# Kernel optimization log

Measured on AMD Instinct MI355X. Metric: run time of the kernel, lower is better.

The kernel has to match this reference:

```python
import jax, jax.numpy as jnp
import numpy as np


def _dwconv3d(x, w, b):
    # depthwise Conv3d, kernel 3, stride 1, padding 1 (SAME), groups = channels
    groups = x.shape[1]
    y = jax.lax.conv_general_dilated(
        x, w, window_strides=(1, 1, 1), padding='SAME',
        feature_group_count=groups,
        dimension_numbers=('NCDHW', 'OIDHW', 'NCDHW'))
    return y + b[None, :, None, None, None]


def setup_inputs() -> dict:
    key = jax.random.key(0)
    ks = jax.random.split(key, 8)
    B, C, K, D, H, W = 4, 64, 64, 16, 64, 64
    sc = 0.1
    return {
        'x_q': jax.random.normal(ks[0], (B, C, D, H, W), jnp.float32),
        'x_kv': jax.random.normal(ks[1], (B, K, D, H, W), jnp.float32),
        'wq': jax.random.normal(ks[2], (C, 1, 3, 3, 3), jnp.float32) * sc,
        'bq': jax.random.normal(ks[3], (C,), jnp.float32) * sc,
        'wk': jax.random.normal(ks[4], (K, 1, 3, 3, 3), jnp.float32) * sc,
        'bk': jax.random.normal(ks[5], (K,), jnp.float32) * sc,
        'wv': jax.random.normal(ks[6], (K, 1, 3, 3, 3), jnp.float32) * sc,
        'bv': jax.random.normal(ks[7], (K,), jnp.float32) * sc,
    }


def reference(x_q, x_kv, wq, bq, wk, bk, wv, bv):
    q = _dwconv3d(x_q, wq, bq)   # [B,C,D,H,W]
    k = _dwconv3d(x_kv, wk, bk)  # [B,K,D,H,W]
    v = _dwconv3d(x_kv, wv, bv)  # [B,K,D,H,W]
    B, C = q.shape[:2]
    K = k.shape[1]
    qf = q.reshape(B, C, -1)     # [B,C,S]
    kf = k.reshape(B, K, -1)     # [B,K,S]
    vf = v.reshape(B, K, -1)     # [B,K,S]
    attn = jnp.einsum('bcs,bks->bck', qf, kf) / jnp.sqrt(jnp.asarray(K, qf.dtype))
    attn = jax.nn.softmax(attn, axis=-1)           # [B,C,K]
    n = int(0.1 * C)
    at = attn.transpose(0, 2, 1)                   # [B,K,C]
    _, idx = jax.lax.top_k(at, n)                  # [B,K,n] indices into C
    mask = jnp.sum(jax.nn.one_hot(idx, C, dtype=attn.dtype), axis=-2)  # [B,K,C]
    attn_m = attn * mask.transpose(0, 2, 1)        # [B,C,K], NOT renormalized
    out = jnp.einsum('bck,bks->bcs', attn_m, vf).reshape(q.shape)
    return x_q + out, attn_m
```

## Files before the change

### kernel.cpp

```cpp
#include <hip/hip_runtime.h>
#include <math.h>

#define BB   4
#define CC   64
#define KK   64
#define DDim 16
#define HDim 64
#define WDim 64
#define SS   (DDim*HDim*WDim)
#define PLANE (HDim*WDim)
#define NCH2 64
#define TOPN 6
#define RSTR 68
#define RROWS 18
#define NSTG 288

typedef __attribute__((ext_vector_type(8))) short bf16x8;
typedef __attribute__((ext_vector_type(4))) float f32x4;

__device__ __forceinline__ unsigned cvt_pk_bf16(float lo, float hi) {
    unsigned r;
    asm("v_cvt_pk_bf16_f32 %0, %1, %2" : "=v"(r) : "v"(lo), "v"(hi));
    return r;
}
__device__ __forceinline__ float bf2f(unsigned short u) {
    union { unsigned u; float f; } v; v.u = ((unsigned)u) << 16; return v.f;
}

__global__ __launch_bounds__(128) void conv_hp4(
    const float* __restrict__ xq, const float* __restrict__ xkv,
    const float* __restrict__ wq, const float* __restrict__ bq,
    const float* __restrict__ wk, const float* __restrict__ bk,
    const float* __restrict__ wv, const float* __restrict__ bv,
    unsigned short* __restrict__ qo, unsigned short* __restrict__ ko,
    unsigned short* __restrict__ vo)
{
    __shared__ float ring[4][RROWS*RSTR];

    int bid  = blockIdx.x;
    int work = (bid & 7) * 256 + (bid >> 3);
    int t  = work >> 10;
    int b  = (work >> 8) & 3;
    int c  = (work >> 2) & 63;
    int hs = work & 3;
    int g0 = hs << 4;

    const float* src = (t ? xkv : xq) + (size_t)(b*CC + c) * SS;
    float wA[27], wB[27], bA, bB;
    if (t == 0) {
        #pragma unroll
        for (int i = 0; i < 27; ++i) { wA[i] = wq[c*27 + i]; wB[i] = 0.f; }
        bA = bq[c]; bB = 0.f;
    } else {
        #pragma unroll
        for (int i = 0; i < 27; ++i) { wA[i] = wk[c*27 + i]; wB[i] = wv[c*27 + i]; }
        bA = bk[c]; bB = bv[c];
    }
    unsigned short* dA = (t ? ko : qo) + (size_t)(b*CC + c) * SS;
    unsigned short* dB = vo + (size_t)(b*CC + c) * SS;

    const int tid  = threadIdx.x;
    const int lane = tid & 63;
    const int wg   = tid & 7;
    const int w0   = wg << 3;
    const int hl   = tid >> 3;
    const int y    = g0 + hl;

    float4 stg[3];
#define SLOAD(p) {                                                             \
    const int p_ = (p);                                                        \
    const bool pv_ = (p_ >= 0 && p_ < DDim);                                   \
    _Pragma("unroll")                                                          \
    for (int i_ = 0; i_ < 3; ++i_) {                                           \
        const int fidx_ = i_*128 + tid;                                        \
        const int row_  = fidx_ >> 4;                                          \
        const int gy_   = g0 - 1 + row_;                                       \
        float4 v_ = make_float4(0.f,0.f,0.f,0.f);                              \
        if (pv_ && fidx_ < NSTG && gy_ >= 0 && gy_ < HDim)                     \
            v_ = *(const float4*)(src + (size_t)p_*PLANE + gy_*WDim            \
                                  + (fidx_ & 15)*4);                           \
        stg[i_] = v_;                                                          \
    } }
#define SWRITE(p) {                                                            \
    float* R_ = ring[(p) & 3];                                                 \
    _Pragma("unroll")                                                          \
    for (int i_ = 0; i_ < 3; ++i_) {                                           \
        const int fidx_ = i_*128 + tid;                                        \
        if (fidx_ < NSTG)                                                      \
            *(float4*)&R_[(fidx_ >> 4)*RSTR + (fidx_ & 15)*4] = stg[i_];       \
    } }

#define COMPUTE_D(dd, DOB) {                                                   \
    float accA[8], accB[8];                                                    \
    _Pragma("unroll")                                                          \
    for (int j = 0; j < 8; ++j) { accA[j] = bA; accB[j] = bB; }                \
    _Pragma("unroll")                                                          \
    for (int dz = 0; dz < 3; ++dz) {                                           \
        const float* R = ring[((dd) + dz + 3) & 3];         \
        _Pragma("unroll")                                                      \
        for (int dy = 0; dy < 3; ++dy) {                                       \
            const int base_ = (hl + dy)*RSTR;                                  \
            float4 a0 = *(const float4*)&R[base_ + w0];                        \
            float4 a1 = *(const float4*)&R[base_ + w0 + 4];                    \
            float lh = __shfl(a1.w, lane - 1, 64);        \
            float rh = __shfl(a0.x, lane + 1, 64);       \
            float r[10];                                                       \
            r[0] = wg       ? lh : 0.f;                                        \
            r[9] = (wg < 7) ? rh : 0.f;                                        \
            r[1]=a0.x; r[2]=a0.y; r[3]=a0.z; r[4]=a0.w;                        \
            r[5]=a1.x; r[6]=a1.y; r[7]=a1.z; r[8]=a1.w;                        \
            const float ca0 = wA[dz*9 + dy*3 + 0];                             \
            const float ca1 = wA[dz*9 + dy*3 + 1];                             \
            const float ca2 = wA[dz*9 + dy*3 + 2];                             \
            const float cb0 = wB[dz*9 + dy*3 + 0];                             \
            const float cb1 = wB[dz*9 + dy*3 + 1];                             \
            const float cb2 = wB[dz*9 + dy*3 + 2];                             \
            _Pragma("unroll")                                                  \
            for (int j = 0; j < 8; ++j) {                                      \
                float sA = fmaf(ca0, r[j],   accA[j]);                         \
                sA       = fmaf(ca1, r[j+1], sA);                              \
                accA[j]  = fmaf(ca2, r[j+2], sA);                              \
                if (DOB) {                                                     \
                    float sB = fmaf(cb0, r[j],   accB[j]);                     \
                    sB       = fmaf(cb1, r[j+1], sB);                          \
                    accB[j]  = fmaf(cb2, r[j+2], sB);                          \
                }                                                              \
            }                                                                  \
        }                                                                      \
    }                                                                          \
    const int off = (dd)*PLANE + y*WDim + w0;                                  \
    uint2 pkA;                                                                 \
    pkA.x = cvt_pk_bf16(accA[0], accA[1]);                                     \
    pkA.y = cvt_pk_bf16(accA[2], accA[3]);                                     \
    uint2 pkA2;                                                                \
    pkA2.x = cvt_pk_bf16(accA[4], accA[5]);                                    \
    pkA2.y = cvt_pk_bf16(accA[6], accA[7]);                                    \
    *(uint2*)&dA[off]     = pkA;                                               \
    *(uint2*)&dA[off + 4] = pkA2;                                              \
    if (DOB) {                                                                 \
        uint2 pkB, pkB2;                                                       \
        pkB.x  = cvt_pk_bf16(accB[0], accB[1]);                                \
        pkB.y  = cvt_pk_bf16(accB[2], accB[3]);                                \
        pkB2.x = cvt_pk_bf16(accB[4], accB[5]);                                \
        pkB2.y = cvt_pk_bf16(accB[6], accB[7]);                                \
        *(uint2*)&dB[off]     = pkB;                                           \
        *(uint2*)&dB[off + 4] = pkB2;                                          \
    } }

    SLOAD(-1); SWRITE(-1);
    SLOAD(0);  SWRITE(0);
    SLOAD(1);  SWRITE(1);
    __syncthreads();

    if (t == 0) {
        for (int d = 0; d < DDim; ++d) {
            if (d < DDim - 1) SLOAD(d + 2);
            COMPUTE_D(d, 0);
            if (d < DDim - 1) SWRITE(d + 2);
            __syncthreads();
        }
    } else {
        for (int d = 0; d < DDim; ++d) {
            if (d < DDim - 1) SLOAD(d + 2);
            COMPUTE_D(d, 1);
            if (d < DDim - 1) SWRITE(d + 2);
            __syncthreads();
        }
    }
#undef SLOAD
#undef SWRITE
#undef COMPUTE_D
}

__global__ __launch_bounds__(256) void gemm1_mfma(
    const unsigned short* __restrict__ qb, const unsigned short* __restrict__ kb,
    float* __restrict__ part)
{
    __shared__ unsigned short lq[64*136];
    __shared__ unsigned short lk[64*136];

    int bid   = blockIdx.x;
    int b     = bid >> 6;
    int chunk = bid & 63;
    int tid   = threadIdx.x;
    int lane  = tid & 63;
    int wid   = tid >> 6;
    int c0    = wid << 4;
    int lr    = lane & 15;
    int kq    = lane >> 4;

    const unsigned short* qsrc = qb + (size_t)b*CC*SS;
    const unsigned short* ksrc = kb + (size_t)b*KK*SS;

    f32x4 acc[4];
    #pragma unroll
    for (int j = 0; j < 4; ++j) acc[j] = (f32x4){0.f, 0.f, 0.f, 0.f};

    const int sbase = chunk << 10;
    for (int sc = 0; sc < 8; ++sc) {
        const int s0 = sbase + (sc << 7);
        __syncthreads();
        #pragma unroll
        for (int it = 0; it < 8; ++it) {
            const int idx  = it*256 + tid;
            const int tile = idx >> 10;
            const int row  = (idx >> 4) & 63;
            const int ch8  = idx & 15;
            const unsigned short* s_ = (tile ? ksrc : qsrc) + (size_t)row*SS + s0 + ch8*8;
            unsigned short* d_ = (tile ? lk : lq) + row*136 + ch8*8;
            *(uint4*)d_ = *(const uint4*)s_;
        }
        __syncthreads();
        #pragma unroll
        for (int ss = 0; ss < 4; ++ss) {
            const int scol = ss*32 + kq*8;
            bf16x8 a = *(const bf16x8*)&lq[(c0 + lr)*136 + scol];
            #pragma unroll
            for (int j = 0; j < 4; ++j) {
                bf16x8 bv = *(const bf16x8*)&lk[(j*16 + lr)*136 + scol];
                acc[j] = __builtin_amdgcn_mfma_f32_16x16x32_bf16(a, bv, acc[j], 0, 0, 0);
            }
        }
    }

    float* pb = part + ((size_t)(b*NCH2 + chunk)) * (CC*KK);
    #pragma unroll
    for (int j = 0; j < 4; ++j)
        #pragma unroll
        for (int r = 0; r < 4; ++r)
            pb[(c0 + kq*4 + r)*KK + j*16 + lr] = acc[j][r];
}

__global__ __launch_bounds__(256) void reduce_attn(
    const float* __restrict__ part, float* __restrict__ attn)
{
    int bid = blockIdx.x;
    int b = bid >> 6, c = bid & 63;
    int tid = threadIdx.x;
    int k = tid & 63, g = tid >> 6;
    float s = 0.f;
    for (int ch = g; ch < NCH2; ch += 4)
        s += part[(size_t)(b*NCH2 + ch)*(CC*KK) + c*KK + k];
    __shared__ float red[256];
    red[tid] = s;
    __syncthreads();
    if (tid < 64) {
        float tot = red[tid] + red[tid+64] + red[tid+128] + red[tid+192];
        attn[b*CC*KK + c*KK + tid] = tot * 0.125f;
    }
}

__global__ __launch_bounds__(64) void softmax_topk(
    const float* __restrict__ attn, float* __restrict__ attn_m)
{
    __shared__ float p[64*65];
    int b = blockIdx.x;
    int t = threadIdx.x;
    for (int i = 0; i < 64; ++i) p[i*65 + t] = attn[b*4096 + i*64 + t];
    __syncthreads();
    float m = -1e30f;
    for (int k = 0; k < 64; ++k) m = fmaxf(m, p[t*65 + k]);
    float sum = 0.f;
    for (int k = 0; k < 64; ++k) { float e = expf(p[t*65+k] - m); p[t*65+k] = e; sum += e; }
    float inv = 1.f / sum;
    for (int k = 0; k < 64; ++k) p[t*65+k] *= inv;
    __syncthreads();
    unsigned long long chosen = 0ull;
    #pragma unroll
    for (int pass = 0; pass < TOPN; ++pass) {
        float best = -1.f; int bi = 0;
        for (int c2 = 0; c2 < 64; ++c2) {
            float v = p[c2*65 + t];
            if (!((chosen >> c2) & 1ull) && v > best) { best = v; bi = c2; }
        }
        chosen |= 1ull << bi;
    }
    for (int c2 = 0; c2 < 64; ++c2) {
        float v = p[c2*65 + t];
        attn_m[b*4096 + c2*64 + t] = ((chosen >> c2) & 1ull) ? v : 0.f;
    }
}

__global__ __launch_bounds__(256) void gemm2_out(
    const float* __restrict__ attn_m, const unsigned short* __restrict__ v,
    const float* __restrict__ xq, float* __restrict__ out)
{
    __shared__ float amt[64][68];
    __shared__ float vt[64][132];
    int bid = blockIdx.x;
    int b  = bid >> 7;
    int ch = bid & 127;
    int tid = threadIdx.x;
    for (int i = 0; i < 16; ++i) {
        int idx = i*256 + tid;
        amt[idx & 63][idx >> 6] = attn_m[b*4096 + idx];
    }
    int c0 = (tid >> 4) * 4;
    int s0 = (tid & 15) * 8;
    const unsigned short* vb = v + (size_t)b*KK*SS;
    const float* xb = xq + (size_t)b*CC*SS;
    float* ob = out + (size_t)b*CC*SS;
    int sb0 = ch * 512;
    for (int st = 0; st < 4; ++st) {
        int sb = sb0 + st*128;
        __syncthreads();
        #pragma unroll
        for (int i = 0; i < 4; ++i) {
            int idx = i*256 + tid;
            int k   = idx >> 4;
            int s8  = (idx & 15) * 8;
            uint4 pk = *(const uint4*)&vb[(size_t)k*SS + sb + s8];
            float* dst = &vt[k][s8];
            dst[0] = bf2f((unsigned short)(pk.x & 0xffff));
            dst[1] = bf2f((unsigned short)(pk.x >> 16));
            dst[2] = bf2f((unsigned short)(pk.y & 0xffff));
            dst[3] = bf2f((unsigned short)(pk.y >> 16));
            dst[4] = bf2f((unsigned short)(pk.z & 0xffff));
            dst[5] = bf2f((unsigned short)(pk.z >> 16));
            dst[6] = bf2f((unsigned short)(pk.w & 0xffff));
            dst[7] = bf2f((unsigned short)(pk.w >> 16));
        }
        __syncthreads();
        float acc[4][8] = {};
        #pragma unroll 8
        for (int k = 0; k < 64; ++k) {
            float4 a  = *(const float4*)&amt[k][c0];
            float4 v0 = *(const float4*)&vt[k][s0];
            float4 v1 = *(const float4*)&vt[k][s0+4];
            float av[4] = {a.x,a.y,a.z,a.w};
            float vv[8] = {v0.x,v0.y,v0.z,v0.w,v1.x,v1.y,v1.z,v1.w};
            #pragma unroll
            for (int i = 0; i < 4; ++i)
                #pragma unroll
                for (int j = 0; j < 8; ++j)
                    acc[i][j] = fmaf(av[i], vv[j], acc[i][j]);
        }
        #pragma unroll
        for (int i = 0; i < 4; ++i) {
            int off = (c0+i)*SS + sb + s0;
            float4 x0 = *(const float4*)&xb[off];
            float4 x1 = *(const float4*)&xb[off+4];
            *(float4*)&ob[off]   = make_float4(acc[i][0]+x0.x, acc[i][1]+x0.y,
                                               acc[i][2]+x0.z, acc[i][3]+x0.w);
            *(float4*)&ob[off+4] = make_float4(acc[i][4]+x1.x, acc[i][5]+x1.y,
                                               acc[i][6]+x1.z, acc[i][7]+x1.w);
        }
    }
}

extern "C" void kernel_launch(void* const* d_in, const int* in_sizes, int n_in,
                              void* d_out, int out_size, void* d_ws, size_t ws_size,
                              hipStream_t stream)
{
    const float* xq  = (const float*)d_in[0];
    const float* xkv = (const float*)d_in[1];
    const float* wq  = (const float*)d_in[2];
    const float* bq  = (const float*)d_in[3];
    const float* wk  = (const float*)d_in[4];
    const float* bk  = (const float*)d_in[5];
    const float* wv  = (const float*)d_in[6];
    const float* bv  = (const float*)d_in[7];
    float* out = (float*)d_out;

    unsigned short* k_ws = (unsigned short*)d_ws;
    unsigned short* v_ws = k_ws + (size_t)BB*KK*SS;
    float* part = (float*)(v_ws + (size_t)BB*KK*SS);
    float* attn = part + (size_t)BB*NCH2*CC*KK;

    unsigned short* q_bf = (unsigned short*)out;
    float* attn_m = out + (size_t)BB*CC*SS;

    conv_hp4   <<<2*BB*CC*4, 128, 0, stream>>>(xq, xkv, wq, bq, wk, bk, wv, bv,
                                               q_bf, k_ws, v_ws);
    gemm1_mfma <<<BB*NCH2,   256, 0, stream>>>(q_bf, k_ws, part);
    reduce_attn<<<BB*CC,     256, 0, stream>>>(part, attn);
    softmax_topk<<<BB,        64, 0, stream>>>(attn, attn_m);
    gemm2_out  <<<BB*128,    256, 0, stream>>>(attn_m, v_ws, xq, out);
}
```

Measured before the change: 146.2 us.

## Merge Q and KV depthwise conv blocks into one uniform block per tile

Each block now convolves both the x_q and x_kv tiles for the same (b, c, h-slab), producing q, k and v together. This replaces the two block types of different cost, where q blocks did one conv and kv blocks did two, with one uniform block that halves the grid and balances work across blocks. In exchange it doubles the LDS ring per block and raises register pressure from the three accumulators and three weight sets, which may lower occupancy. It also issues wider 16-byte bf16 stores.

After: 139.9 us (median of 2 runs). 4.3% less time.

```diff
diff --git a/kernel.cpp b/kernel.cpp
--- a/kernel.cpp
+++ b/kernel.cpp
@@ -27,7 +27,7 @@
     union { unsigned u; float f; } v; v.u = ((unsigned)u) << 16; return v.f;
 }
 
-__global__ __launch_bounds__(128) void conv_hp4(
+__global__ __launch_bounds__(128) void conv_uni(
     const float* __restrict__ xq, const float* __restrict__ xkv,
     const float* __restrict__ wq, const float* __restrict__ bq,
     const float* __restrict__ wk, const float* __restrict__ bk,
@@ -35,29 +35,30 @@
     unsigned short* __restrict__ qo, unsigned short* __restrict__ ko,
     unsigned short* __restrict__ vo)
 {
-    __shared__ float ring[4][RROWS*RSTR];
+    __shared__ float ringQ[4][RROWS*RSTR];
+    __shared__ float ringK[4][RROWS*RSTR];
 
     int bid  = blockIdx.x;
-    int work = (bid & 7) * 256 + (bid >> 3);
-    int t  = work >> 10;
-    int b  = (work >> 8) & 3;
+    int work = (bid & 7) * 128 + (bid >> 3);
+    int b  = work >> 8;
     int c  = (work >> 2) & 63;
-    int hs = work & 3;
-    int g0 = hs << 4;
-
-    const float* src = (t ? xkv : xq) + (size_t)(b*CC + c) * SS;
-    float wA[27], wB[27], bA, bB;
-    if (t == 0) {
-        #pragma unroll
-        for (int i = 0; i < 27; ++i) { wA[i] = wq[c*27 + i]; wB[i] = 0.f; }
-        bA = bq[c]; bB = 0.f;
-    } else {
-        #pragma unroll
-        for (int i = 0; i < 27; ++i) { wA[i] = wk[c*27 + i]; wB[i] = wv[c*27 + i]; }
-        bA = bk[c]; bB = bv[c];
-    }
-    unsigned short* dA = (t ? ko : qo) + (size_t)(b*CC + c) * SS;
-    unsigned short* dB = vo + (size_t)(b*CC + c) * SS;
+    int hq = work & 3;
+    int g0 = hq << 4;
+
+    const float* srcQ = xq  + (size_t)(b*CC + c) * SS;
+    const float* srcK = xkv + (size_t)(b*CC + c) * SS;
+    float wQ[27], wK[27], wV[27];
+    #pragma unroll
+    for (int i = 0; i < 27; ++i) {
+        wQ[i] = wq[c*27 + i];
+        wK[i] = wk[c*27 + i];
+        wV[i] = wv[c*27 + i];
+    }
+    const float bQ = bq[c], bK = bk[c], bV = bv[c];
+
+    unsigned short* dQ = qo + (size_t)(b*CC + c) * SS;
+    unsigned short* dK = ko + (size_t)(b*CC + c) * SS;
+    unsigned short* dV = vo + (size_t)(b*CC + c) * SS;
 
     const int tid  = threadIdx.x;
     const int lane = tid & 63;
@@ -66,8 +67,8 @@
     const int hl   = tid >> 3;
     const int y    = g0 + hl;
 
-    float4 stg[3];
-#define SLOAD(p) {                                                             \
+    float4 stgQ[3], stgK[3];
+#define SLOAD2(p) {                                                            \
     const int p_ = (p);                                                        \
     const bool pv_ = (p_ >= 0 && p_ < DDim);                                   \
     _Pragma("unroll")                                                          \
@@ -75,100 +76,110 @@
         const int fidx_ = i_*128 + tid;                                        \
         const int row_  = fidx_ >> 4;                                          \
         const int gy_   = g0 - 1 + row_;                                       \
-        float4 v_ = make_float4(0.f,0.f,0.f,0.f);                              \
-        if (pv_ && fidx_ < NSTG && gy_ >= 0 && gy_ < HDim)                     \
-            v_ = *(const float4*)(src + (size_t)p_*PLANE + gy_*WDim            \
-                                  + (fidx_ & 15)*4);                           \
-        stg[i_] = v_;                                                          \
+        float4 vq_ = make_float4(0.f,0.f,0.f,0.f), vk_ = vq_;                  \
+        if (pv_ && fidx_ < NSTG && gy_ >= 0 && gy_ < HDim) {                   \
+            const size_t o_ = (size_t)p_*PLANE + gy_*WDim + (fidx_ & 15)*4;    \
+            vq_ = *(const float4*)(srcQ + o_);                                 \
+            vk_ = *(const float4*)(srcK + o_);                                 \
+        }                                                                      \
+        stgQ[i_] = vq_; stgK[i_] = vk_;                                        \
     } }
-#define SWRITE(p) {                                                            \
-    float* R_ = ring[(p) & 3];                                                 \
+#define SWRITE2(p) {                                                           \
+    float* RQ_ = ringQ[(p) & 3];                                               \
+    float* RK_ = ringK[(p) & 3];                                               \
     _Pragma("unroll")                                                          \
     for (int i_ = 0; i_ < 3; ++i_) {                                           \
         const int fidx_ = i_*128 + tid;                                        \
-        if (fidx_ < NSTG)                                                      \
-            *(float4*)&R_[(fidx_ >> 4)*RSTR + (fidx_ & 15)*4] = stg[i_];       \
+        if (fidx_ < NSTG) {                                                    \
+            const int off_ = (fidx_ >> 4)*RSTR + (fidx_ & 15)*4;               \
+            *(float4*)&RQ_[off_] = stgQ[i_];                                   \
+            *(float4*)&RK_[off_] = stgK[i_];                                   \
+        }                                                                      \
     } }
 
-#define COMPUTE_D(dd, DOB) {                                                   \
-    float accA[8], accB[8];                                                    \
+#define COMPUTE_D(dd) {                                                        \
+    float accQ[8], accK[8], accV[8];                                           \
     _Pragma("unroll")                                                          \
-    for (int j = 0; j < 8; ++j) { accA[j] = bA; accB[j] = bB; }                \
+    for (int j = 0; j < 8; ++j) { accQ[j] = bQ; accK[j] = bK; accV[j] = bV; }  \
     _Pragma("unroll")                                                          \
     for (int dz = 0; dz < 3; ++dz) {                                           \
-        const float* R = ring[((dd) + dz + 3) & 3];         \
+        const float* RQ = ringQ[((dd) + dz + 3) & 3];       \
+        const float* RK = ringK[((dd) + dz + 3) & 3];                          \
         _Pragma("unroll")                                                      \
         for (int dy = 0; dy < 3; ++dy) {                                       \
             const int base_ = (hl + dy)*RSTR;                                  \
-            float4 a0 = *(const float4*)&R[base_ + w0];                        \
-            float4 a1 = *(const float4*)&R[base_ + w0 + 4];                    \
-            float lh = __shfl(a1.w, lane - 1, 64);        \
-            float rh = __shfl(a0.x, lane + 1, 64);       \
-            float r[10];                                                       \
-            r[0] = wg       ? lh : 0.f;                                        \
-            r[9] = (wg < 7) ? rh : 0.f;                                        \
-            r[1]=a0.x; r[2]=a0.y; r[3]=a0.z; r[4]=a0.w;                        \
-            r[5]=a1.x; r[6]=a1.y; r[7]=a1.z; r[8]=a1.w;                        \
-            const float ca0 = wA[dz*9 + dy*3 + 0];                             \
-            const float ca1 = wA[dz*9 + dy*3 + 1];                             \
-            const float ca2 = wA[dz*9 + dy*3 + 2];                             \
-            const float cb0 = wB[dz*9 + dy*3 + 0];                             \
-            const float cb1 = wB[dz*9 + dy*3 + 1];                             \
-            const float cb2 = wB[dz*9 + dy*3 + 2];                             \
+            float4 qa0 = *(const float4*)&RQ[base_ + w0];                      \
+            float4 qa1 = *(const float4*)&RQ[base_ + w0 + 4];                  \
+            float4 ka0 = *(const float4*)&RK[base_ + w0];                      \
+            float4 ka1 = *(const float4*)&RK[base_ + w0 + 4];                  \
+            float qlh = __shfl(qa1.w, lane - 1, 64);                           \
+            float qrh = __shfl(qa0.x, lane + 1, 64);                           \
+            float klh = __shfl(ka1.w, lane - 1, 64);                           \
+            float krh = __shfl(ka0.x, lane + 1, 64);                           \
+            float rq[10], rk[10];                                              \
+            rq[0] = wg       ? qlh : 0.f;                                      \
+            rq[9] = (wg < 7) ? qrh : 0.f;                                      \
+            rq[1]=qa0.x; rq[2]=qa0.y; rq[3]=qa0.z; rq[4]=qa0.w;                \
+            rq[5]=qa1.x; rq[6]=qa1.y; rq[7]=qa1.z; rq[8]=qa1.w;                \
+            rk[0] = wg       ? klh : 0.f;                                      \
+            rk[9] = (wg < 7) ? krh : 0.f;                                      \
+            rk[1]=ka0.x; rk[2]=ka0.y; rk[3]=ka0.z; rk[4]=ka0.w;                \
+            rk[5]=ka1.x; rk[6]=ka1.y; rk[7]=ka1.z; rk[8]=ka1.w;                \
+            const float cq0 = wQ[dz*9 + dy*3 + 0];                             \
+            const float cq1 = wQ[dz*9 + dy*3 + 1];                             \
+            const float cq2 = wQ[dz*9 + dy*3 + 2];                             \
+            const float ck0 = wK[dz*9 + dy*3 + 0];                             \
+            const float ck1 = wK[dz*9 + dy*3 + 1];                             \
+            const float ck2 = wK[dz*9 + dy*3 + 2];                             \
+            const float cv0 = wV[dz*9 + dy*3 + 0];                             \
+            const float cv1 = wV[dz*9 + dy*3 + 1];                             \
+            const float cv2 = wV[dz*9 + dy*3 + 2];                             \
             _Pragma("unroll")                                                  \
             for (int j = 0; j < 8; ++j) {                                      \
-                float sA = fmaf(ca0, r[j],   accA[j]);                         \
-                sA       = fmaf(ca1, r[j+1], sA);                              \
-                accA[j]  = fmaf(ca2, r[j+2], sA);                              \
-                if (DOB) {                                                     \
-                    float sB = fmaf(cb0, r[j],   accB[j]);                     \
-                    sB       = fmaf(cb1, r[j+1], sB);                          \
-                    accB[j]  = fmaf(cb2, r[j+2], sB);                          \
-                }                                                              \
+                float sQ = fmaf(cq0, rq[j],   accQ[j]);                        \
+                sQ       = fmaf(cq1, rq[j+1], sQ);                             \
+                accQ[j]  = fmaf(cq2, rq[j+2], sQ);                             \
+                float sK = fmaf(ck0, rk[j],   accK[j]);                        \
+                sK       = fmaf(ck1, rk[j+1], sK);                             \
+                accK[j]  = fmaf(ck2, rk[j+2], sK);                             \
+                float sV = fmaf(cv0, rk[j],   accV[j]);                        \
+                sV       = fmaf(cv1, rk[j+1], sV);                             \
+                accV[j]  = fmaf(cv2, rk[j+2], sV);                             \
             }                                                                  \
         }                                                                      \
     }                                                                          \
     const int off = (dd)*PLANE + y*WDim + w0;                                  \
-    uint2 pkA;                                                                 \
-    pkA.x = cvt_pk_bf16(accA[0], accA[1]);                                     \
-    pkA.y = cvt_pk_bf16(accA[2], accA[3]);                                     \
-    uint2 pkA2;                                                                \
-    pkA2.x = cvt_pk_bf16(accA[4], accA[5]);                                    \
-    pkA2.y = cvt_pk_bf16(accA[6], accA[7]);                                    \
-    *(uint2*)&dA[off]     = pkA;                                               \
-    *(uint2*)&dA[off + 4] = pkA2;                                              \
-    if (DOB) {                                                                 \
-        uint2 pkB, pkB2;                                                       \
-        pkB.x  = cvt_pk_bf16(accB[0], accB[1]);                                \
-        pkB.y  = cvt_pk_bf16(accB[2], accB[3]);                                \
-        pkB2.x = cvt_pk_bf16(accB[4], accB[5]);                                \
-        pkB2.y = cvt_pk_bf16(accB[6], accB[7]);                                \
-        *(uint2*)&dB[off]     = pkB;                                           \
-        *(uint2*)&dB[off + 4] = pkB2;                                          \
-    } }
-
-    SLOAD(-1); SWRITE(-1);
-    SLOAD(0);  SWRITE(0);
-    SLOAD(1);  SWRITE(1);
+    uint4 pq, pk, pv;                                                          \
+    pq.x = cvt_pk_bf16(accQ[0], accQ[1]);                                      \
+    pq.y = cvt_pk_bf16(accQ[2], accQ[3]);                                      \
+    pq.z = cvt_pk_bf16(accQ[4], accQ[5]);                                      \
+    pq.w = cvt_pk_bf16(accQ[6], accQ[7]);                                      \
+    pk.x = cvt_pk_bf16(accK[0], accK[1]);                                      \
+    pk.y = cvt_pk_bf16(accK[2], accK[3]);                                      \
+    pk.z = cvt_pk_bf16(accK[4], accK[5]);                                      \
+    pk.w = cvt_pk_bf16(accK[6], accK[7]);                                      \
+    pv.x = cvt_pk_bf16(accV[0], accV[1]);                                      \
+    pv.y = cvt_pk_bf16(accV[2], accV[3]);                                      \
+    pv.z = cvt_pk_bf16(accV[4], accV[5]);                                      \
+    pv.w = cvt_pk_bf16(accV[6], accV[7]);                                      \
+    *(uint4*)&dQ[off] = pq;                                                    \
+    *(uint4*)&dK[off] = pk;                                                    \
+    *(uint4*)&dV[off] = pv;                                                    \
+    }
+
+    SLOAD2(-1); SWRITE2(-1);
+    SLOAD2(0);  SWRITE2(0);
+    SLOAD2(1);  SWRITE2(1);
     __syncthreads();
 
-    if (t == 0) {
-        for (int d = 0; d < DDim; ++d) {
-            if (d < DDim - 1) SLOAD(d + 2);
-            COMPUTE_D(d, 0);
-            if (d < DDim - 1) SWRITE(d + 2);
-            __syncthreads();
-        }
-    } else {
-        for (int d = 0; d < DDim; ++d) {
-            if (d < DDim - 1) SLOAD(d + 2);
-            COMPUTE_D(d, 1);
-            if (d < DDim - 1) SWRITE(d + 2);
-            __syncthreads();
-        }
-    }
-#undef SLOAD
-#undef SWRITE
+    for (int d = 0; d < DDim; ++d) {
+        if (d < DDim - 1) SLOAD2(d + 2);
+        COMPUTE_D(d);
+        if (d < DDim - 1) SWRITE2(d + 2);
+        __syncthreads();
+    }
+#undef SLOAD2
+#undef SWRITE2
 #undef COMPUTE_D
 }
 
@@ -370,7 +381,7 @@
     unsigned short* q_bf = (unsigned short*)out;
     float* attn_m = out + (size_t)BB*CC*SS;
 
-    conv_hp4   <<<2*BB*CC*4, 128, 0, stream>>>(xq, xkv, wq, bq, wk, bk, wv, bv,
+    conv_uni   <<<BB*CC*4,   128, 0, stream>>>(xq, xkv, wq, bq, wk, bk, wv, bv,
                                                q_bf, k_ws, v_ws);
     gemm1_mfma <<<BB*NCH2,   256, 0, stream>>>(q_bf, k_ws, part);
     reduce_attn<<<BB*CC,     256, 0, stream>>>(part, attn);
```
